# Kernel tuning notes

Measured on AMD Instinct MI355X. Metric: run time of the kernel, lower is better.

## Reference

```python
import jax, jax.numpy as jnp
import numpy as np

BLOCK = 64  # quantization block size along in_features
IN, OUT, RANK, ALPHA = 4096, 4096, 16, 32
SCALING = ALPHA / RANK


def setup_inputs() -> dict:
    key = jax.random.key(0)
    ks = jax.random.split(key, 6)
    x = jax.random.normal(ks[0], (8, 1024, IN), dtype=jnp.float32)
    # int4 codes in [0, 15]; dequant subtracts 8 -> [-8, 7]
    qweight = jax.random.randint(ks[1], (OUT, IN), 0, 16, dtype=jnp.int32)
    # blockwise absmax-style scales, small positive
    scales = jax.random.uniform(ks[2], (OUT, IN // BLOCK), dtype=jnp.float32) * 0.02 + 1e-3
    bias = jax.random.normal(ks[3], (OUT,), dtype=jnp.float32) * 0.02
    lora_A = jax.random.normal(ks[4], (IN, RANK), dtype=jnp.float32) * 0.02
    lora_B = jnp.zeros((RANK, OUT), dtype=jnp.float32)
    return {"x": x, "qweight": qweight, "scales": scales, "bias": bias,
            "lora_A": lora_A, "lora_B": lora_B}


def _dequant(qweight, scales):
    # qweight: [out, in] int codes in [0,15]; scales: [out, in/BLOCK]
    out, in_f = qweight.shape
    q = (qweight.astype(jnp.float32) - 8.0).reshape(out, in_f // BLOCK, BLOCK)
    return (q * scales[:, :, None]).reshape(out, in_f)  # [out, in]


def reference(x, qweight, scales, bias, lora_A, lora_B):
    W = _dequant(qweight, scales)                      # [out, in]
    base = jnp.einsum('bsi,oi->bso', x, W) + bias      # quantized linear
    lora = jnp.einsum('bsr,ro->bso', jnp.einsum('bsi,ir->bsr', x, lora_A), lora_B)
    return base + lora * SCALING
```

## Files before the change

### kernel.cpp

```cpp
#include <hip/hip_runtime.h>
#include <hip/hip_bf16.h>

#define IN_F 4096
#define OUT_F 4096
#define M_TOK 8192
#define RANK 16

#define CONV_BLOCKS (M_TOK * IN_F / (8 * 256))
#define DEQ_BLOCKS  2048

typedef __attribute__((ext_vector_type(4))) float f32x4;
typedef __attribute__((ext_vector_type(8))) short short8;

struct alignas(16) bf16x8_s { __hip_bfloat16 v[8]; };

__global__ __launch_bounds__(256) void prep_kernel(
    const float* __restrict__ x,
    const int* __restrict__ q,
    const float* __restrict__ scales,
    const float* __restrict__ lA,
    const float* __restrict__ lB,
    __hip_bfloat16* __restrict__ xb,
    __hip_bfloat16* __restrict__ W) {
    const int tid = threadIdx.x;

    if (blockIdx.x < CONV_BLOCKS) {
        size_t base = ((size_t)blockIdx.x * 256 + tid) * 8;
        float4 v0 = *(const float4*)(x + base);
        float4 v1 = *(const float4*)(x + base + 4);
        bf16x8_s r;
        r.v[0] = __float2bfloat16(v0.x);
        r.v[1] = __float2bfloat16(v0.y);
        r.v[2] = __float2bfloat16(v0.z);
        r.v[3] = __float2bfloat16(v0.w);
        r.v[4] = __float2bfloat16(v1.x);
        r.v[5] = __float2bfloat16(v1.y);
        r.v[6] = __float2bfloat16(v1.z);
        r.v[7] = __float2bfloat16(v1.w);
        *(bf16x8_s*)(xb + base) = r;
        return;
    }

    const int bid = blockIdx.x - CONV_BLOCKS;
    const int o0 = (bid >> 1) * 4;
    const int i0 = (bid & 1) * 2048 + tid * 8;

    float bw[16][4];
#pragma unroll
    for (int r = 0; r < 16; ++r)
#pragma unroll
        for (int oi = 0; oi < 4; ++oi)
            bw[r][oi] = 2.0f * lB[(size_t)r * OUT_F + o0 + oi];

    float fold[4][8];
#pragma unroll
    for (int e = 0; e < 8; ++e) {
        const float* ar = lA + (size_t)(i0 + e) * RANK;
        float4 a0 = *(const float4*)(ar + 0);
        float4 a1 = *(const float4*)(ar + 4);
        float4 a2 = *(const float4*)(ar + 8);
        float4 a3 = *(const float4*)(ar + 12);
#pragma unroll
        for (int oi = 0; oi < 4; ++oi) {
            float f = a0.x * bw[0][oi] + a0.y * bw[1][oi]
                    + a0.z * bw[2][oi] + a0.w * bw[3][oi]
                    + a1.x * bw[4][oi] + a1.y * bw[5][oi]
                    + a1.z * bw[6][oi] + a1.w * bw[7][oi]
                    + a2.x * bw[8][oi] + a2.y * bw[9][oi]
                    + a2.z * bw[10][oi] + a2.w * bw[11][oi]
                    + a3.x * bw[12][oi] + a3.y * bw[13][oi]
                    + a3.z * bw[14][oi] + a3.w * bw[15][oi];
            fold[oi][e] = f;
        }
    }

#pragma unroll
    for (int oi = 0; oi < 4; ++oi) {
        const int o = o0 + oi;
        const float s = scales[o * 64 + (i0 >> 6)];
        const int4* qp = (const int4*)(q + (size_t)o * IN_F + i0);
        int4 q0 = qp[0];
        int4 q1 = qp[1];
        bf16x8_s r;
        r.v[0] = __float2bfloat16(s * (float)(q0.x - 8) + fold[oi][0]);
        r.v[1] = __float2bfloat16(s * (float)(q0.y - 8) + fold[oi][1]);
        r.v[2] = __float2bfloat16(s * (float)(q0.z - 8) + fold[oi][2]);
        r.v[3] = __float2bfloat16(s * (float)(q0.w - 8) + fold[oi][3]);
        r.v[4] = __float2bfloat16(s * (float)(q1.x - 8) + fold[oi][4]);
        r.v[5] = __float2bfloat16(s * (float)(q1.y - 8) + fold[oi][5]);
        r.v[6] = __float2bfloat16(s * (float)(q1.z - 8) + fold[oi][6]);
        r.v[7] = __float2bfloat16(s * (float)(q1.w - 8) + fold[oi][7]);
        *(bf16x8_s*)(W + (size_t)o * IN_F + i0) = r;
    }
}

#define BK 64
#define NT (IN_F / BK)

__device__ __forceinline__ short8 ldfrag(const short* p, int half, int row, int gran) {
    return *(const short8*)(p + half * 8192 + row * 64 + ((gran ^ (row & 7)) * 8));
}

#define STAGE(LDSbuf, SRC, ROW0, K0)                                          \
    {                                                                         \
        _Pragma("unroll")                                                     \
        for (int j = 0; j < 2; ++j) {                                         \
            const __hip_bfloat16* g = (SRC) +                                 \
                (size_t)((ROW0) + j * 64 + wave * 8 + srow) * IN_F + (K0) + sgc; \
            __builtin_amdgcn_global_load_lds(                                 \
                (const __attribute__((address_space(1))) void*)g,             \
                (__attribute__((address_space(3))) void*)((LDSbuf) + (j * 64 + wave * 8) * 64), \
                16, 0, 0);                                                    \
        }                                                                     \
    }

#define PHASE(ABUF, BBUF, MH, NH, READA, STAGE_CODE, WAITCODE)                \
    {                                                                         \
        if (READA) {                                                          \
            _Pragma("unroll") for (int f = 0; f < 4; ++f)                     \
            _Pragma("unroll") for (int kk = 0; kk < 2; ++kk)                  \
                fa[f][kk] = ldfrag(ABUF, MH, wm * 64 + f * 16 + fr, kk * 4 + fc); \
        }                                                                     \
        _Pragma("unroll") for (int f = 0; f < 2; ++f)                         \
        _Pragma("unroll") for (int kk = 0; kk < 2; ++kk)                      \
            fb[f][kk] = ldfrag(BBUF, NH, wn * 32 + f * 16 + fr, kk * 4 + fc); \
        STAGE_CODE;                                                           \
        WAITCODE;                                                             \
        __builtin_amdgcn_s_barrier();                                         \
        asm volatile("s_waitcnt lgkmcnt(0)" ::: "memory");                    \
        __builtin_amdgcn_sched_barrier(0);                                    \
        __builtin_amdgcn_s_setprio(1);                                        \
        _Pragma("unroll") for (int f = 0; f < 4; ++f)                         \
        _Pragma("unroll") for (int g2 = 0; g2 < 2; ++g2)                      \
        _Pragma("unroll") for (int kk = 0; kk < 2; ++kk)                      \
            acc[(MH) * 4 + f][(NH) * 2 + g2] =                                \
                __builtin_amdgcn_mfma_f32_16x16x32_bf16(                      \
                    fa[f][kk], fb[g2][kk], acc[(MH) * 4 + f][(NH) * 2 + g2], 0, 0, 0); \
        __builtin_amdgcn_s_setprio(0);                                        \
        __builtin_amdgcn_s_barrier();                                         \
    }

__global__ __launch_bounds__(512, 2) void qlora_gemm_kernel(
    const __hip_bfloat16* __restrict__ xb,
    const __hip_bfloat16* __restrict__ Wq,
    const float* __restrict__ bias,
    float* __restrict__ out) {
    __shared__ __hip_bfloat16 As[2][16384];
    __shared__ __hip_bfloat16 Bs[2][16384];

    const int tid  = threadIdx.x;
    const int wave = tid >> 6;
    const int lane = tid & 63;
    const int wm = wave >> 2;
    const int wn = wave & 3;

    const int wg = ((int)blockIdx.x & 7) * 64 + ((int)blockIdx.x >> 3);
    const int bx = wg & 15;
    const int by = wg >> 4;
    const int m0 = by * 256;
    const int n0 = bx * 256;

    f32x4 acc[8][4];
#pragma unroll
    for (int i = 0; i < 8; ++i)
#pragma unroll
        for (int j = 0; j < 4; ++j)
            acc[i][j] = (f32x4){0.f, 0.f, 0.f, 0.f};

    const int srow = lane >> 3;
    const int sgc  = ((lane & 7) ^ srow) * 8;

    const int fr = lane & 15;
    const int fc = lane >> 4;

    const short* A0p = (const short*)As[0];
    const short* A1p = (const short*)As[1];
    const short* B0p = (const short*)Bs[0];
    const short* B1p = (const short*)Bs[1];

    short8 fa[4][2];
    short8 fb[2][2];

    STAGE(As[0],        xb, m0,       0);
    STAGE(Bs[0],        Wq, n0,       0);
    STAGE(As[0] + 8192, xb, m0 + 128, 0);
    STAGE(Bs[0] + 8192, Wq, n0 + 128, 0);
    STAGE(As[1],        xb, m0,       BK);
    STAGE(Bs[1],        Wq, n0,       BK);
    asm volatile("s_waitcnt vmcnt(4)" ::: "memory");
    __builtin_amdgcn_s_barrier();

    for (int it = 0; it < NT / 2; ++it) {
        const int t = it * 2;
        const int k_t1 = ((t + 1) & (NT - 1)) * BK;
        const int k_t2 = ((t + 2) & (NT - 1)) * BK;
        const int k_t3 = ((t + 3) & (NT - 1)) * BK;

        PHASE(A0p, B0p, 0, 0, 1, STAGE(As[1] + 8192, xb, m0 + 128, k_t1), );
        PHASE(A0p, B0p, 0, 1, 0, STAGE(Bs[1] + 8192, Wq, n0 + 128, k_t1), );
        PHASE(A0p, B0p, 1, 0, 1, STAGE(As[0],        xb, m0,       k_t2), );
        PHASE(A0p, B0p, 1, 1, 0, STAGE(Bs[0],        Wq, n0,       k_t2),
              asm volatile("s_waitcnt vmcnt(4)" ::: "memory"));

        PHASE(A1p, B1p, 0, 0, 1, STAGE(As[0] + 8192, xb, m0 + 128, k_t2), );
        PHASE(A1p, B1p, 0, 1, 0, STAGE(Bs[0] + 8192, Wq, n0 + 128, k_t2), );
        PHASE(A1p, B1p, 1, 0, 1, STAGE(As[1],        xb, m0,       k_t3), );
        PHASE(A1p, B1p, 1, 1, 0, STAGE(Bs[1],        Wq, n0,       k_t3),
              asm volatile("s_waitcnt vmcnt(4)" ::: "memory"));
    }

    asm volatile("s_waitcnt vmcnt(0)" ::: "memory");

    const int cc  = lane & 15;
    const int rr4 = (lane >> 4) * 4;
    float bv[2][2];
#pragma unroll
    for (int nh = 0; nh < 2; ++nh)
#pragma unroll
        for (int fn = 0; fn < 2; ++fn)
            bv[nh][fn] = bias[n0 + nh * 128 + wn * 32 + fn * 16 + cc];

#pragma unroll
    for (int mh = 0; mh < 2; ++mh)
#pragma unroll
        for (int fm = 0; fm < 4; ++fm) {
            const int m = m0 + mh * 128 + wm * 64 + fm * 16 + rr4;
#pragma unroll
            for (int nh = 0; nh < 2; ++nh)
#pragma unroll
                for (int fn = 0; fn < 2; ++fn) {
                    const int n = n0 + nh * 128 + wn * 32 + fn * 16 + cc;
                    float* op = out + (size_t)m * OUT_F + n;
                    const f32x4 a = acc[mh * 4 + fm][nh * 2 + fn];
#pragma unroll
                    for (int r = 0; r < 4; ++r)
                        op[(size_t)r * OUT_F] = a[r] + bv[nh][fn];
                }
        }
}

extern "C" void kernel_launch(void* const* d_in, const int* in_sizes, int n_in,
                              void* d_out, int out_size, void* d_ws, size_t ws_size,
                              hipStream_t stream) {
    const float* x      = (const float*)d_in[0];
    const int*   qw     = (const int*)  d_in[1];
    const float* scales = (const float*)d_in[2];
    const float* bias   = (const float*)d_in[3];
    const float* lA     = (const float*)d_in[4];
    const float* lB     = (const float*)d_in[5];
    float* out = (float*)d_out;

    char* ws = (char*)d_ws;
    __hip_bfloat16* Wq = (__hip_bfloat16*)ws;
    __hip_bfloat16* xb = (__hip_bfloat16*)(ws + (size_t)32 * 1024 * 1024);

    prep_kernel<<<CONV_BLOCKS + DEQ_BLOCKS, 256, 0, stream>>>(
        x, qw, scales, lA, lB, xb, Wq);
    qlora_gemm_kernel<<<dim3(512), dim3(512), 0, stream>>>(xb, Wq, bias, out);
}
```

Before: 618.6 us.

## Split prep into conv and dequant kernels; reorganize GEMM warp tiling over K halves

The fused prep kernel becomes two launches: a grid-stride fp32-to-bf16 conversion of x over fewer blocks, and a separate dequant/LoRA-fold kernel. In the GEMM, each wave now covers a contiguous 64-column N slice instead of two 32-column halves. Phases iterate over K sub-steps, so B fragments are loaded once per K half and reused across both M halves. This cuts LDS fragment reads and changes the staging schedule (two stages issued together in the last phase). It adds an extra kernel launch and shifts when global loads are issued relative to the vmcnt waits.

```diff
diff --git a/kernel.cpp b/kernel.cpp
--- a/kernel.cpp
+++ b/kernel.cpp
@@ -6,26 +6,22 @@
 #define M_TOK 8192
 #define RANK 16
 
-#define CONV_BLOCKS (M_TOK * IN_F / (8 * 256))
-#define DEQ_BLOCKS  2048
-
 typedef __attribute__((ext_vector_type(4))) float f32x4;
 typedef __attribute__((ext_vector_type(8))) short short8;
 
 struct alignas(16) bf16x8_s { __hip_bfloat16 v[8]; };
 
-__global__ __launch_bounds__(256) void prep_kernel(
+#define CONV_BLOCKS 2048
+#define CONV_ITERS (M_TOK * IN_F / (8 * 256 * CONV_BLOCKS))
+
+__global__ __launch_bounds__(256) void conv_kernel(
     const float* __restrict__ x,
-    const int* __restrict__ q,
-    const float* __restrict__ scales,
-    const float* __restrict__ lA,
-    const float* __restrict__ lB,
-    __hip_bfloat16* __restrict__ xb,
-    __hip_bfloat16* __restrict__ W) {
-    const int tid = threadIdx.x;
-
-    if (blockIdx.x < CONV_BLOCKS) {
-        size_t base = ((size_t)blockIdx.x * 256 + tid) * 8;
+    __hip_bfloat16* __restrict__ xb) {
+    size_t idx = (size_t)blockIdx.x * 256 + threadIdx.x;
+    const size_t stride = (size_t)CONV_BLOCKS * 256;
+#pragma unroll
+    for (int it = 0; it < CONV_ITERS; ++it, idx += stride) {
+        const size_t base = idx * 8;
         float4 v0 = *(const float4*)(x + base);
         float4 v1 = *(const float4*)(x + base + 4);
         bf16x8_s r;
@@ -38,10 +34,19 @@
         r.v[6] = __float2bfloat16(v1.z);
         r.v[7] = __float2bfloat16(v1.w);
         *(bf16x8_s*)(xb + base) = r;
-        return;
-    }
-
-    const int bid = blockIdx.x - CONV_BLOCKS;
+    }
+}
+
+#define DEQ_BLOCKS 2048
+
+__global__ __launch_bounds__(256) void deq_kernel(
+    const int* __restrict__ q,
+    const float* __restrict__ scales,
+    const float* __restrict__ lA,
+    const float* __restrict__ lB,
+    __hip_bfloat16* __restrict__ W) {
+    const int tid = threadIdx.x;
+    const int bid = blockIdx.x;
     const int o0 = (bid >> 1) * 4;
     const int i0 = (bid & 1) * 2048 + tid * 8;
 
@@ -114,16 +119,14 @@
         }                                                                     \
     }
 
-#define PHASE(ABUF, BBUF, MH, NH, READA, STAGE_CODE, WAITCODE)                \
+#define PHASE(ABUF, BBUF, MH, KK, READB, STAGE_CODE, WAITCODE)                \
     {                                                                         \
-        if (READA) {                                                          \
-            _Pragma("unroll") for (int f = 0; f < 4; ++f)                     \
-            _Pragma("unroll") for (int kk = 0; kk < 2; ++kk)                  \
-                fa[f][kk] = ldfrag(ABUF, MH, wm * 64 + f * 16 + fr, kk * 4 + fc); \
+        _Pragma("unroll") for (int f = 0; f < 4; ++f)                         \
+            fa[f] = ldfrag(ABUF, MH, wm * 64 + f * 16 + fr, (KK) * 4 + fc);   \
+        if (READB) {                                                          \
+            _Pragma("unroll") for (int g2 = 0; g2 < 4; ++g2)                  \
+                fb[g2] = ldfrag(BBUF, bhalf, brow0 + g2 * 16 + fr, (KK) * 4 + fc); \
         }                                                                     \
-        _Pragma("unroll") for (int f = 0; f < 2; ++f)                         \
-        _Pragma("unroll") for (int kk = 0; kk < 2; ++kk)                      \
-            fb[f][kk] = ldfrag(BBUF, NH, wn * 32 + f * 16 + fr, kk * 4 + fc); \
         STAGE_CODE;                                                           \
         WAITCODE;                                                             \
         __builtin_amdgcn_s_barrier();                                         \
@@ -131,11 +134,10 @@
         __builtin_amdgcn_sched_barrier(0);                                    \
         __builtin_amdgcn_s_setprio(1);                                        \
         _Pragma("unroll") for (int f = 0; f < 4; ++f)                         \
-        _Pragma("unroll") for (int g2 = 0; g2 < 2; ++g2)                      \
-        _Pragma("unroll") for (int kk = 0; kk < 2; ++kk)                      \
-            acc[(MH) * 4 + f][(NH) * 2 + g2] =                                \
+        _Pragma("unroll") for (int g2 = 0; g2 < 4; ++g2)                      \
+            acc[(MH) * 4 + f][g2] =                                           \
                 __builtin_amdgcn_mfma_f32_16x16x32_bf16(                      \
-                    fa[f][kk], fb[g2][kk], acc[(MH) * 4 + f][(NH) * 2 + g2], 0, 0, 0); \
+                    fa[f], fb[g2], acc[(MH) * 4 + f][g2], 0, 0, 0);           \
         __builtin_amdgcn_s_setprio(0);                                        \
         __builtin_amdgcn_s_barrier();                                         \
     }
@@ -173,13 +175,16 @@
     const int fr = lane & 15;
     const int fc = lane >> 4;
 
+    const int bhalf = wn >> 1;
+    const int brow0 = (wn & 1) * 64;
+
     const short* A0p = (const short*)As[0];
     const short* A1p = (const short*)As[1];
     const short* B0p = (const short*)Bs[0];
     const short* B1p = (const short*)Bs[1];
 
-    short8 fa[4][2];
-    short8 fb[2][2];
+    short8 fa[4];
+    short8 fb[4];
 
     STAGE(As[0],        xb, m0,       0);
     STAGE(Bs[0],        Wq, n0,       0);
@@ -197,15 +202,17 @@
         const int k_t3 = ((t + 3) & (NT - 1)) * BK;
 
         PHASE(A0p, B0p, 0, 0, 1, STAGE(As[1] + 8192, xb, m0 + 128, k_t1), );
-        PHASE(A0p, B0p, 0, 1, 0, STAGE(Bs[1] + 8192, Wq, n0 + 128, k_t1), );
-        PHASE(A0p, B0p, 1, 0, 1, STAGE(As[0],        xb, m0,       k_t2), );
-        PHASE(A0p, B0p, 1, 1, 0, STAGE(Bs[0],        Wq, n0,       k_t2),
+        PHASE(A0p, B0p, 1, 0, 0, STAGE(Bs[1] + 8192, Wq, n0 + 128, k_t1), );
+        PHASE(A0p, B0p, 0, 1, 1, , );
+        PHASE(A0p, B0p, 1, 1, 0,
+              { STAGE(As[0], xb, m0, k_t2); STAGE(Bs[0], Wq, n0, k_t2); },
               asm volatile("s_waitcnt vmcnt(4)" ::: "memory"));
 
         PHASE(A1p, B1p, 0, 0, 1, STAGE(As[0] + 8192, xb, m0 + 128, k_t2), );
-        PHASE(A1p, B1p, 0, 1, 0, STAGE(Bs[0] + 8192, Wq, n0 + 128, k_t2), );
-        PHASE(A1p, B1p, 1, 0, 1, STAGE(As[1],        xb, m0,       k_t3), );
-        PHASE(A1p, B1p, 1, 1, 0, STAGE(Bs[1],        Wq, n0,       k_t3),
+        PHASE(A1p, B1p, 1, 0, 0, STAGE(Bs[0] + 8192, Wq, n0 + 128, k_t2), );
+        PHASE(A1p, B1p, 0, 1, 1, , );
+        PHASE(A1p, B1p, 1, 1, 0,
+              { STAGE(As[1], xb, m0, k_t3); STAGE(Bs[1], Wq, n0, k_t3); },
               asm volatile("s_waitcnt vmcnt(4)" ::: "memory"));
     }
 
@@ -213,29 +220,25 @@
 
     const int cc  = lane & 15;
     const int rr4 = (lane >> 4) * 4;
-    float bv[2][2];
-#pragma unroll
-    for (int nh = 0; nh < 2; ++nh)
-#pragma unroll
-        for (int fn = 0; fn < 2; ++fn)
-            bv[nh][fn] = bias[n0 + nh * 128 + wn * 32 + fn * 16 + cc];
+    float bv[4];
+#pragma unroll
+    for (int g2 = 0; g2 < 4; ++g2)
+        bv[g2] = bias[n0 + wn * 64 + g2 * 16 + cc];
 
 #pragma unroll
     for (int mh = 0; mh < 2; ++mh)
 #pragma unroll
-        for (int fm = 0; fm < 4; ++fm) {
-            const int m = m0 + mh * 128 + wm * 64 + fm * 16 + rr4;
-#pragma unroll
-            for (int nh = 0; nh < 2; ++nh)
-#pragma unroll
-                for (int fn = 0; fn < 2; ++fn) {
-                    const int n = n0 + nh * 128 + wn * 32 + fn * 16 + cc;
-                    float* op = out + (size_t)m * OUT_F + n;
-                    const f32x4 a = acc[mh * 4 + fm][nh * 2 + fn];
-#pragma unroll
-                    for (int r = 0; r < 4; ++r)
-                        op[(size_t)r * OUT_F] = a[r] + bv[nh][fn];
-                }
+        for (int f = 0; f < 4; ++f) {
+            const int m = m0 + mh * 128 + wm * 64 + f * 16 + rr4;
+#pragma unroll
+            for (int g2 = 0; g2 < 4; ++g2) {
+                const int n = n0 + wn * 64 + g2 * 16 + cc;
+                float* op = out + (size_t)m * OUT_F + n;
+                const f32x4 a = acc[mh * 4 + f][g2];
+#pragma unroll
+                for (int r = 0; r < 4; ++r)
+                    op[(size_t)r * OUT_F] = a[r] + bv[g2];
+            }
         }
 }
 
@@ -254,7 +257,7 @@
     __hip_bfloat16* Wq = (__hip_bfloat16*)ws;
     __hip_bfloat16* xb = (__hip_bfloat16*)(ws + (size_t)32 * 1024 * 1024);
 
-    prep_kernel<<<CONV_BLOCKS + DEQ_BLOCKS, 256, 0, stream>>>(
-        x, qw, scales, lA, lB, xb, Wq);
+    conv_kernel<<<CONV_BLOCKS, 256, 0, stream>>>(x, xb);
+    deq_kernel<<<DEQ_BLOCKS, 256, 0, stream>>>(qw, scales, lA, lB, Wq);
     qlora_gemm_kernel<<<dim3(512), dim3(512), 0, stream>>>(xb, Wq, bias, out);
 }
```

Measured after the change: 594.1 us. -4.0%, faster.
